# Performance work log

Measured on AMD Instinct MI355X. Metric: run time of the kernel, lower is better.

The kernel has to match this reference:

```python
import jax, jax.numpy as jnp
import numpy as np
from jax import lax

C = 96          # channels (d_model)
D_STATE = 16
D_CONV = 4
EXPAND = 2
D_INNER = EXPAND * C          # 192
DT_RANK = (C + 15) // 16      # 6 (ceil(d_model/16), mamba_ssm default)
B, H, W = 4, 96, 96
LN_EPS = 1e-5


def setup_inputs() -> dict:
    key = jax.random.key(0)
    ks = jax.random.split(key, 10)
    s = 0.02
    return {
        "spatial_feat": jax.random.normal(ks[0], (B, C, H, W), jnp.float32),
        "freq_feat":    jax.random.normal(ks[1], (B, C, H, W), jnp.float32),
        # fusion proj: nn.Linear(2C, C) with bias
        "proj_w": jax.random.normal(ks[2], (C, 2 * C), jnp.float32) * s,
        "proj_b": jnp.zeros((C,), jnp.float32),
        # Mamba params (mamba_ssm defaults: in/x/out proj bias=False, conv bias=True)
        "in_proj_w": jax.random.normal(ks[3], (2 * D_INNER, C), jnp.float32) * s,
        "conv_w": jax.random.normal(ks[4], (D_INNER, 1, D_CONV), jnp.float32) * s,
        "conv_b": jnp.zeros((D_INNER,), jnp.float32),
        "x_proj_w": jax.random.normal(ks[5], (DT_RANK + 2 * D_STATE, D_INNER), jnp.float32) * s,
        "dt_proj_w": jax.random.normal(ks[6], (D_INNER, DT_RANK), jnp.float32) * s,
        "dt_proj_b": jnp.full((D_INNER,), -4.6, jnp.float32),  # softplus ~ 0.01
        "A_log": jnp.log(jnp.tile(jnp.arange(1, D_STATE + 1, dtype=jnp.float32), (D_INNER, 1))),
        "D_param": jnp.ones((D_INNER,), jnp.float32),
        "out_proj_w": jax.random.normal(ks[7], (C, D_INNER), jnp.float32) * s,
        "ln_g": jnp.ones((C,), jnp.float32),
        "ln_b": jnp.zeros((C,), jnp.float32),
    }


def _mamba_fusion(spatial_feat, freq_feat, proj_w, proj_b, in_proj_w, conv_w,
                  conv_b, x_proj_w, dt_proj_w, dt_proj_b, A_log, D_param,
                  out_proj_w, ln_g, ln_b):
    Bsz, Ch, Hh, Ww = spatial_feat.shape
    L = Hh * Ww
    # concat + flatten(2).transpose(1,2): [B, L, 2C]
    seq = jnp.concatenate([spatial_feat, freq_feat], axis=1).reshape(Bsz, 2 * Ch, L).transpose(0, 2, 1)
    x = seq @ proj_w.T + proj_b  # [B, L, C]

    # ---- Mamba mixer ----
    xz = x @ in_proj_w.T                      # [B, L, 2*d_inner]
    x_in, z = jnp.split(xz, 2, axis=-1)
    # causal depthwise conv1d over sequence
    xc = lax.conv_general_dilated(
        x_in.transpose(0, 2, 1), conv_w, (1,), [(D_CONV - 1, 0)],
        dimension_numbers=('NCH', 'OIH', 'NCH'), feature_group_count=D_INNER)
    xc = jax.nn.silu(xc + conv_b[None, :, None]).transpose(0, 2, 1)  # [B, L, d_inner]

    x_dbl = xc @ x_proj_w.T                   # [B, L, dt_rank + 2*d_state]
    dt, Bm, Cm = jnp.split(x_dbl, [DT_RANK, DT_RANK + D_STATE], axis=-1)
    delta = jax.nn.softplus(dt @ dt_proj_w.T + dt_proj_b)  # [B, L, d_inner]
    A = -jnp.exp(A_log)                       # [d_inner, d_state]

    def step(h, inp):
        d_t, B_t, C_t, x_t = inp              # [B,d_in],[B,ds],[B,ds],[B,d_in]
        h = jnp.exp(d_t[:, :, None] * A) * h + (d_t * x_t)[:, :, None] * B_t[:, None, :]
        y_t = jnp.einsum('bds,bs->bd', h, C_t)
        return h, y_t

    xs = (delta.transpose(1, 0, 2), Bm.transpose(1, 0, 2),
          Cm.transpose(1, 0, 2), xc.transpose(1, 0, 2))
    h0 = jnp.zeros((Bsz, D_INNER, D_STATE), x.dtype)
    _, ys = lax.scan(step, h0, xs)            # ys: [L, B, d_inner]
    y = ys.transpose(1, 0, 2) + xc * D_param
    y = y * jax.nn.silu(z)
    mixed = y @ out_proj_w.T                  # [B, L, C]

    # LayerNorm over channel dim
    mu = mixed.mean(-1, keepdims=True)
    var = mixed.var(-1, keepdims=True)
    normed = (mixed - mu) * lax.rsqrt(var + LN_EPS) * ln_g + ln_b

    fused = normed.transpose(0, 2, 1).reshape(Bsz, Ch, Hh, Ww)
    return fused + spatial_feat


def reference(spatial_feat, freq_feat, proj_w, proj_b, in_proj_w, conv_w,
              conv_b, x_proj_w, dt_proj_w, dt_proj_b, A_log, D_param,
              out_proj_w, ln_g, ln_b):
    return _mamba_fusion(spatial_feat, freq_feat, proj_w, proj_b, in_proj_w,
                         conv_w, conv_b, x_proj_w, dt_proj_w, dt_proj_b,
                         A_log, D_param, out_proj_w, ln_g, ln_b)
```

## Files before the change

### kernel.cpp

```cpp
#include <hip/hip_runtime.h>
#include <math.h>

#define kC    96
#define kL    9216
#define kB    4
#define kDI   192
#define kDS   16
#define kDTR  6
#define kCL   128
#define kNC   72
#define kNROW (kB*kL)
#define kNSEQ (kB*kDI*kDS)

__device__ __forceinline__ float silu_f(float v) { return v / (1.f + expf(-v)); }

__global__ __launch_bounds__(256)
void k0_prep(const float* __restrict__ proj_w, const float* __restrict__ proj_b,
             const float* __restrict__ in_proj_w, const float* __restrict__ A_log,
             float* __restrict__ WcT, float* __restrict__ bias_c, float* __restrict__ A)
{
    int idx = blockIdx.x * 256 + threadIdx.x;
    if (idx < 384 * 192) {
        int co = idx / 192;
        int k  = idx % 192;
        float acc = 0.f;
        #pragma unroll 4
        for (int c = 0; c < 96; ++c)
            acc += in_proj_w[co * 96 + c] * proj_w[c * 192 + k];
        WcT[k * 384 + co] = acc;
    }
    if (idx < 384) {
        float acc = 0.f;
        for (int c = 0; c < 96; ++c) acc += in_proj_w[idx * 96 + c] * proj_b[c];
        bias_c[idx] = acc;
    }
    if (idx < kDI * kDS) {
        A[idx] = -expf(A_log[idx]);
    }
}

__global__ __launch_bounds__(384)
void k1_xz(const float* __restrict__ spatial, const float* __restrict__ freq,
           const float* __restrict__ WcT, const float* __restrict__ bias_c,
           float* __restrict__ x_in, float* __restrict__ z)
{
    __shared__ float sq[192 * 16];
    const int t   = threadIdx.x;
    const int blk = blockIdx.x;
    const int b   = blk / (kL / 16);
    const int l0  = (blk % (kL / 16)) * 16;

    #pragma unroll
    for (int i = 0; i < 8; ++i) {
        int e  = i * 384 + t;
        int k  = e >> 4, li = e & 15;
        float v;
        if (k < 96) v = spatial[(size_t)(b * 96 + k) * kL + l0 + li];
        else        v = freq   [(size_t)(b * 96 + (k - 96)) * kL + l0 + li];
        sq[e] = v;
    }
    __syncthreads();

    const int co = t;
    float acc[16];
    {
        float bc = bias_c[co];
        #pragma unroll
        for (int i = 0; i < 16; ++i) acc[i] = bc;
    }
    const float4* sq4 = (const float4*)sq;
    const float* wp = WcT + co;
    for (int k = 0; k < 192; ++k) {
        float w = wp[k * 384];
        float4 a0 = sq4[k * 4 + 0];
        float4 a1 = sq4[k * 4 + 1];
        float4 a2 = sq4[k * 4 + 2];
        float4 a3 = sq4[k * 4 + 3];
        acc[0]  += w * a0.x;  acc[1]  += w * a0.y;  acc[2]  += w * a0.z;  acc[3]  += w * a0.w;
        acc[4]  += w * a1.x;  acc[5]  += w * a1.y;  acc[6]  += w * a1.z;  acc[7]  += w * a1.w;
        acc[8]  += w * a2.x;  acc[9]  += w * a2.y;  acc[10] += w * a2.z;  acc[11] += w * a2.w;
        acc[12] += w * a3.x;  acc[13] += w * a3.y;  acc[14] += w * a3.z;  acc[15] += w * a3.w;
    }
    const size_t rbase = (size_t)b * kL + l0;
    if (co < 192) {
        #pragma unroll
        for (int li = 0; li < 16; ++li) x_in[(rbase + li) * 192 + co] = acc[li];
    } else {
        #pragma unroll
        for (int li = 0; li < 16; ++li) z[(rbase + li) * 192 + (co - 192)] = acc[li];
    }
}

__global__ __launch_bounds__(256)
void k2_conv(const float* __restrict__ x_in, const float* __restrict__ conv_w,
             const float* __restrict__ conv_b, float* __restrict__ xc)
{
    int idx = blockIdx.x * 256 + threadIdx.x;
    if (idx >= kNROW * 48) return;
    const int d4 = idx % 48;
    const int r  = idx / 48;
    const int l  = r % kL;
    const int d0 = d4 * 4;
    float ax = 0.f, ay = 0.f, az = 0.f, aw = 0.f;
    #pragma unroll
    for (int k = 0; k < 4; ++k) {
        int li = l - 3 + k;
        if (li < 0) continue;
        const float4 xv = *(const float4*)&x_in[(size_t)(r - 3 + k) * 192 + d0];
        ax += xv.x * conv_w[(d0 + 0) * 4 + k];
        ay += xv.y * conv_w[(d0 + 1) * 4 + k];
        az += xv.z * conv_w[(d0 + 2) * 4 + k];
        aw += xv.w * conv_w[(d0 + 3) * 4 + k];
    }
    float4 o;
    o.x = silu_f(ax + conv_b[d0 + 0]);
    o.y = silu_f(ay + conv_b[d0 + 1]);
    o.z = silu_f(az + conv_b[d0 + 2]);
    o.w = silu_f(aw + conv_b[d0 + 3]);
    *(float4*)&xc[(size_t)r * 192 + d0] = o;
}

__global__ __launch_bounds__(256)
void k3_xproj(const float* __restrict__ xc, const float* __restrict__ x_proj_w,
              float* __restrict__ dtr, float* __restrict__ BC)
{
    int idx = blockIdx.x * 256 + threadIdx.x;
    if (idx >= kNROW * 38) return;
    const int j = idx % 38;
    const int r = idx / 38;
    const float4* xr = (const float4*)&xc[(size_t)r * 192];
    const float4* wr = (const float4*)&x_proj_w[j * 192];
    float acc = 0.f;
    #pragma unroll 4
    for (int k4 = 0; k4 < 48; ++k4) {
        float4 a = xr[k4], w = wr[k4];
        acc += a.x * w.x + a.y * w.y + a.z * w.z + a.w * w.w;
    }
    if (j < 6) dtr[(size_t)r * 6 + j] = acc;
    else       BC[(size_t)r * 32 + (j - 6)] = acc;
}

__global__ __launch_bounds__(256)
void k4_dt(const float* __restrict__ dtr, const float* __restrict__ dt_proj_w,
           const float* __restrict__ dt_proj_b, float* __restrict__ delta)
{
    int idx = blockIdx.x * 256 + threadIdx.x;
    if (idx >= kNROW * 192) return;
    const int d = idx % 192;
    const int r = idx / 192;
    float acc = dt_proj_b[d];
    #pragma unroll
    for (int j = 0; j < 6; ++j)
        acc += dtr[(size_t)r * 6 + j] * dt_proj_w[d * 6 + j];
    float sp = (acc > 20.f) ? acc : log1pf(expf(acc));
    delta[(size_t)r * 192 + d] = sp;
}

__global__ __launch_bounds__(256)
void k5_scan1(const float* __restrict__ delta, const float* __restrict__ xc,
              const float* __restrict__ BC, const float* __restrict__ A,
              float* __restrict__ Pc, float* __restrict__ Sc)
{
    const int wid  = (blockIdx.x * 256 + threadIdx.x) >> 6;
    const int lane = threadIdx.x & 63;
    const int c  = wid % kNC;
    const int dg = (wid / kNC) % 48;
    const int b  = wid / (kNC * 48);
    const int s  = lane & 15;
    const int d  = dg * 4 + (lane >> 4);
    const float Ads = A[dg * 64 + lane];

    const size_t rbase = (size_t)b * kL + (size_t)c * kCL;
    const float* dp = delta + rbase * 192 + d;
    const float* xp = xc    + rbase * 192 + d;
    const float* bp = BC    + rbase * 32  + s;

    float P = 1.f, S = 0.f;
    #pragma unroll 4
    for (int i = 0; i < kCL; ++i) {
        float dv = *dp, xv = *xp, bv = *bp;
        float a  = __expf(dv * Ads);
        float bt = dv * xv * bv;
        P *= a;
        S  = a * S + bt;
        dp += 192; xp += 192; bp += 32;
    }
    const int row = (b * 192 + d) * 16 + s;
    Pc[(size_t)c * kNSEQ + row] = P;
    Sc[(size_t)c * kNSEQ + row] = S;
}

__global__ __launch_bounds__(256)
void k6_cscan(const float* __restrict__ Pc, const float* __restrict__ Sc,
              float* __restrict__ hin)
{
    const int row = blockIdx.x * 256 + threadIdx.x;
    float h = 0.f;
    for (int c = 0; c < kNC; ++c) {
        size_t o = (size_t)c * kNSEQ + row;
        hin[o] = h;
        h = Pc[o] * h + Sc[o];
    }
}

__global__ __launch_bounds__(256)
void k7_scan2(const float* __restrict__ delta, const float* __restrict__ xc,
              const float* __restrict__ BC, const float* __restrict__ A,
              const float* __restrict__ hin, float* __restrict__ ys)
{
    const int wid  = (blockIdx.x * 256 + threadIdx.x) >> 6;
    const int lane = threadIdx.x & 63;
    const int c  = wid % kNC;
    const int dg = (wid / kNC) % 48;
    const int b  = wid / (kNC * 48);
    const int s  = lane & 15;
    const int d  = dg * 4 + (lane >> 4);
    const float Ads = A[dg * 64 + lane];
    const int row = (b * 192 + d) * 16 + s;

    const size_t rbase = (size_t)b * kL + (size_t)c * kCL;
    const float* dp = delta + rbase * 192 + d;
    const float* xp = xc    + rbase * 192 + d;
    const float* bp = BC    + rbase * 32  + s;
    const float* cp = BC    + rbase * 32  + 16 + s;
    float*       yp = ys    + rbase * 192 + d;

    float h = hin[(size_t)c * kNSEQ + row];
    for (int i = 0; i < kCL; ++i) {
        float dv = *dp, xv = *xp, bv = *bp, cv = *cp;
        float a = __expf(dv * Ads);
        h = a * h + dv * xv * bv;
        float pv = h * cv;
        pv += __shfl_xor(pv, 1);
        pv += __shfl_xor(pv, 2);
        pv += __shfl_xor(pv, 4);
        pv += __shfl_xor(pv, 8);
        if (s == 0) *yp = pv;
        dp += 192; xp += 192; bp += 32; cp += 32; yp += 192;
    }
}

__global__ __launch_bounds__(256)
void k8_final(const float* __restrict__ ys, const float* __restrict__ xc,
              const float* __restrict__ z, const float* __restrict__ Dp,
              const float* __restrict__ out_proj_w, const float* __restrict__ ln_g,
              const float* __restrict__ ln_b, const float* __restrict__ spatial,
              float* __restrict__ out)
{
    __shared__ float yt[32 * 196];
    __shared__ float wt[96 * 36];
    const int t = threadIdx.x;
    const size_t r0 = (size_t)blockIdx.x * 32;
    const int b = (int)(r0 / kL);

    #pragma unroll
    for (int i = 0; i < 6; ++i) {
        int e  = i * 256 + t;
        int l  = e / 48, d4 = e % 48;
        size_t r = r0 + l;
        float4 yv = *(const float4*)&ys[r * 192 + d4 * 4];
        float4 xv = *(const float4*)&xc[r * 192 + d4 * 4];
        float4 zv = *(const float4*)&z [r * 192 + d4 * 4];
        float4 Dv = *(const float4*)&Dp[d4 * 4];
        float4 o;
        o.x = (yv.x + xv.x * Dv.x) * silu_f(zv.x);
        o.y = (yv.y + xv.y * Dv.y) * silu_f(zv.y);
        o.z = (yv.z + xv.z * Dv.z) * silu_f(zv.z);
        o.w = (yv.w + xv.w * Dv.w) * silu_f(zv.w);
        *(float4*)&yt[l * 196 + d4 * 4] = o;
    }
    __syncthreads();

    const int l  = t >> 3;
    const int cg = t & 7;
    float acc[12];
    #pragma unroll
    for (int i = 0; i < 12; ++i) acc[i] = 0.f;

    for (int kc = 0; kc < 6; ++kc) {
        __syncthreads();
        #pragma unroll
        for (int i = 0; i < 3; ++i) {
            int e = i * 256 + t;
            int c = e / 8, k4 = e % 8;
            float4 w = *(const float4*)&out_proj_w[c * 192 + kc * 32 + k4 * 4];
            *(float4*)&wt[c * 36 + k4 * 4] = w;
        }
        __syncthreads();
        #pragma unroll
        for (int k4 = 0; k4 < 8; ++k4) {
            float4 yv = *(const float4*)&yt[l * 196 + kc * 32 + k4 * 4];
            #pragma unroll
            for (int i = 0; i < 12; ++i) {
                const float4 wv = *(const float4*)&wt[(cg + 8 * i) * 36 + k4 * 4];
                acc[i] += yv.x * wv.x + yv.y * wv.y + yv.z * wv.z + yv.w * wv.w;
            }
        }
    }

    float sum = 0.f, ss = 0.f;
    #pragma unroll
    for (int i = 0; i < 12; ++i) { sum += acc[i]; ss += acc[i] * acc[i]; }
    #pragma unroll
    for (int m = 1; m < 8; m <<= 1) {
        sum += __shfl_xor(sum, m);
        ss  += __shfl_xor(ss, m);
    }
    const float mu  = sum * (1.f / 96.f);
    const float var = ss * (1.f / 96.f) - mu * mu;
    const float rs  = rsqrtf(var + 1e-5f);
    const int lg = (int)(r0 % kL) + l;
    #pragma unroll
    for (int i = 0; i < 12; ++i) {
        int c = cg + 8 * i;
        float nv = (acc[i] - mu) * rs * ln_g[c] + ln_b[c];
        size_t o = ((size_t)b * 96 + c) * kL + lg;
        out[o] = nv + spatial[o];
    }
}

extern "C" void kernel_launch(void* const* d_in, const int* in_sizes, int n_in,
                              void* d_out, int out_size, void* d_ws, size_t ws_size,
                              hipStream_t stream) {
    const float* spatial    = (const float*)d_in[0];
    const float* freq       = (const float*)d_in[1];
    const float* proj_w     = (const float*)d_in[2];
    const float* proj_b     = (const float*)d_in[3];
    const float* in_proj_w  = (const float*)d_in[4];
    const float* conv_w     = (const float*)d_in[5];
    const float* conv_b     = (const float*)d_in[6];
    const float* x_proj_w   = (const float*)d_in[7];
    const float* dt_proj_w  = (const float*)d_in[8];
    const float* dt_proj_b  = (const float*)d_in[9];
    const float* A_log      = (const float*)d_in[10];
    const float* D_param    = (const float*)d_in[11];
    const float* out_proj_w = (const float*)d_in[12];
    const float* ln_g       = (const float*)d_in[13];
    const float* ln_b       = (const float*)d_in[14];
    float* out = (float*)d_out;

    char* wsb = (char*)d_ws;
    size_t off = 0;
    auto alloc = [&](size_t bytes) -> float* {
        float* p = (float*)(wsb + off);
        off += (bytes + 255) & ~(size_t)255;
        return p;
    };
    float* x_in  = alloc((size_t)kNROW * kDI * 4);
    float* z     = alloc((size_t)kNROW * kDI * 4);
    float* xc    = alloc((size_t)kNROW * kDI * 4);
    float* delta = alloc((size_t)kNROW * kDI * 4);
    float* dtr   = alloc((size_t)kNROW * kDTR * 4);
    float* BC    = alloc((size_t)kNROW * 32 * 4);
    float* Pc    = alloc((size_t)kNC * kNSEQ * 4);
    float* Sc    = alloc((size_t)kNC * kNSEQ * 4);
    float* hin   = alloc((size_t)kNC * kNSEQ * 4);
    float* WcT   = alloc((size_t)192 * 384 * 4);
    float* biasc = alloc(384 * 4);
    float* Aa    = alloc((size_t)kDI * kDS * 4);
    float* ys    = x_in;

    k0_prep <<<288,  256, 0, stream>>>(proj_w, proj_b, in_proj_w, A_log, WcT, biasc, Aa);
    k1_xz   <<<2304, 384, 0, stream>>>(spatial, freq, WcT, biasc, x_in, z);
    k2_conv <<<6912, 256, 0, stream>>>(x_in, conv_w, conv_b, xc);
    k3_xproj<<<5472, 256, 0, stream>>>(xc, x_proj_w, dtr, BC);
    k4_dt   <<<27648,256, 0, stream>>>(dtr, dt_proj_w, dt_proj_b, delta);
    k5_scan1<<<3456, 256, 0, stream>>>(delta, xc, BC, Aa, Pc, Sc);
    k6_cscan<<<48,   256, 0, stream>>>(Pc, Sc, hin);
    k7_scan2<<<3456, 256, 0, stream>>>(delta, xc, BC, Aa, hin, ys);
    k8_final<<<1152, 256, 0, stream>>>(ys, xc, z, D_param, out_proj_w, ln_g, ln_b, spatial, out);
}
```

Before: 664.8 us.

## Fuse x_proj and dt_proj kernels and retile the input projection GEMM

Merges the x_proj and dt_proj/softplus kernels into one block-tiled kernel. It stages 64 rows of xc transposed in shared memory, keeps dt_rank values on chip instead of writing a dtr buffer, and reuses the same shared tile to transpose delta for coalesced stores. The k1 input-projection GEMM is retiled to 32 rows per block and 6x8 register accumulators per thread with float4 staging loads, which raises reuse per weight load. Trade-offs: larger shared-memory footprint and far fewer blocks (576) for the fused kernel, which may reduce occupancy and latency hiding.

```diff
diff --git a/kernel.cpp b/kernel.cpp
--- a/kernel.cpp
+++ b/kernel.cpp
@@ -39,55 +39,66 @@
     }
 }
 
-__global__ __launch_bounds__(384)
+__global__ __launch_bounds__(256)
 void k1_xz(const float* __restrict__ spatial, const float* __restrict__ freq,
            const float* __restrict__ WcT, const float* __restrict__ bias_c,
            float* __restrict__ x_in, float* __restrict__ z)
 {
-    __shared__ float sq[192 * 16];
+    __shared__ float As[192 * 36];
     const int t   = threadIdx.x;
     const int blk = blockIdx.x;
-    const int b   = blk / (kL / 16);
-    const int l0  = (blk % (kL / 16)) * 16;
-
-    #pragma unroll
-    for (int i = 0; i < 8; ++i) {
-        int e  = i * 384 + t;
-        int k  = e >> 4, li = e & 15;
-        float v;
-        if (k < 96) v = spatial[(size_t)(b * 96 + k) * kL + l0 + li];
-        else        v = freq   [(size_t)(b * 96 + (k - 96)) * kL + l0 + li];
-        sq[e] = v;
+    const int b   = blk / 288;
+    const int l0  = (blk % 288) * 32;
+
+    #pragma unroll
+    for (int i = 0; i < 6; ++i) {
+        int e  = i * 256 + t;
+        int k  = e >> 3, lg = e & 7;
+        const float* src = (k < 96)
+            ? &spatial[(size_t)(b * 96 + k) * kL]
+            : &freq   [(size_t)(b * 96 + (k - 96)) * kL];
+        float4 v = *(const float4*)&src[l0 + lg * 4];
+        *(float4*)&As[k * 36 + lg * 4] = v;
     }
     __syncthreads();
 
-    const int co = t;
-    float acc[16];
-    {
-        float bc = bias_c[co];
-        #pragma unroll
-        for (int i = 0; i < 16; ++i) acc[i] = bc;
-    }
-    const float4* sq4 = (const float4*)sq;
-    const float* wp = WcT + co;
+    const int w    = t >> 6;
+    const int lane = t & 63;
+    float acc[6][8];
+    #pragma unroll
+    for (int i = 0; i < 6; ++i) {
+        float bc = bias_c[lane + 64 * i];
+        #pragma unroll
+        for (int l = 0; l < 8; ++l) acc[i][l] = bc;
+    }
+
+    const float* wp = WcT + lane;
+    #pragma unroll 2
     for (int k = 0; k < 192; ++k) {
-        float w = wp[k * 384];
-        float4 a0 = sq4[k * 4 + 0];
-        float4 a1 = sq4[k * 4 + 1];
-        float4 a2 = sq4[k * 4 + 2];
-        float4 a3 = sq4[k * 4 + 3];
-        acc[0]  += w * a0.x;  acc[1]  += w * a0.y;  acc[2]  += w * a0.z;  acc[3]  += w * a0.w;
-        acc[4]  += w * a1.x;  acc[5]  += w * a1.y;  acc[6]  += w * a1.z;  acc[7]  += w * a1.w;
-        acc[8]  += w * a2.x;  acc[9]  += w * a2.y;  acc[10] += w * a2.z;  acc[11] += w * a2.w;
-        acc[12] += w * a3.x;  acc[13] += w * a3.y;  acc[14] += w * a3.z;  acc[15] += w * a3.w;
-    }
-    const size_t rbase = (size_t)b * kL + l0;
-    if (co < 192) {
-        #pragma unroll
-        for (int li = 0; li < 16; ++li) x_in[(rbase + li) * 192 + co] = acc[li];
-    } else {
-        #pragma unroll
-        for (int li = 0; li < 16; ++li) z[(rbase + li) * 192 + (co - 192)] = acc[li];
+        const float4 a0 = *(const float4*)&As[k * 36 + w * 8];
+        const float4 a1 = *(const float4*)&As[k * 36 + w * 8 + 4];
+        float wv[6];
+        #pragma unroll
+        for (int i = 0; i < 6; ++i) wv[i] = wp[k * 384 + 64 * i];
+        #pragma unroll
+        for (int i = 0; i < 6; ++i) {
+            acc[i][0] += wv[i] * a0.x;  acc[i][1] += wv[i] * a0.y;
+            acc[i][2] += wv[i] * a0.z;  acc[i][3] += wv[i] * a0.w;
+            acc[i][4] += wv[i] * a1.x;  acc[i][5] += wv[i] * a1.y;
+            acc[i][6] += wv[i] * a1.z;  acc[i][7] += wv[i] * a1.w;
+        }
+    }
+
+    const size_t rbase = (size_t)b * kL + l0 + w * 8;
+    #pragma unroll
+    for (int l = 0; l < 8; ++l) {
+        const size_t ro = (rbase + l) * 192;
+        #pragma unroll
+        for (int i = 0; i < 3; ++i)
+            x_in[ro + lane + 64 * i] = acc[i][l];
+        #pragma unroll
+        for (int i = 3; i < 6; ++i)
+            z[ro + lane + 64 * i - 192] = acc[i][l];
     }
 }
 
@@ -121,39 +132,93 @@
 }
 
 __global__ __launch_bounds__(256)
-void k3_xproj(const float* __restrict__ xc, const float* __restrict__ x_proj_w,
-              float* __restrict__ dtr, float* __restrict__ BC)
-{
-    int idx = blockIdx.x * 256 + threadIdx.x;
-    if (idx >= kNROW * 38) return;
-    const int j = idx % 38;
-    const int r = idx / 38;
-    const float4* xr = (const float4*)&xc[(size_t)r * 192];
-    const float4* wr = (const float4*)&x_proj_w[j * 192];
-    float acc = 0.f;
+void k34(const float* __restrict__ xc, const float* __restrict__ x_proj_w,
+         const float* __restrict__ dt_proj_w, const float* __restrict__ dt_proj_b,
+         float* __restrict__ BC, float* __restrict__ delta)
+{
+    __shared__ float xcT[192 * 65];
+    __shared__ float bc_s[64 * 33];
+    __shared__ float dtr_s[64 * 9];
+    const int t = threadIdx.x;
+    const size_t R0 = (size_t)blockIdx.x * 64;
+
+    #pragma unroll
+    for (int i = 0; i < 12; ++i) {
+        int e = i * 256 + t;
+        int r = e / 48, k4 = e % 48;
+        float4 v = *(const float4*)&xc[(R0 + r) * 192 + k4 * 4];
+        xcT[(k4 * 4 + 0) * 65 + r] = v.x;
+        xcT[(k4 * 4 + 1) * 65 + r] = v.y;
+        xcT[(k4 * 4 + 2) * 65 + r] = v.z;
+        xcT[(k4 * 4 + 3) * 65 + r] = v.w;
+    }
+    __syncthreads();
+
+    const int lane = t & 63;
+    const int w = __builtin_amdgcn_readfirstlane(t >> 6);
+
+    float acc[10];
+    #pragma unroll
+    for (int i = 0; i < 10; ++i) acc[i] = 0.f;
+    int jj[10];
+    #pragma unroll
+    for (int i = 0; i < 10; ++i) { int j = w + 4 * i; jj[i] = (j < 38) ? j : 37; }
+
     #pragma unroll 4
-    for (int k4 = 0; k4 < 48; ++k4) {
-        float4 a = xr[k4], w = wr[k4];
-        acc += a.x * w.x + a.y * w.y + a.z * w.z + a.w * w.w;
-    }
-    if (j < 6) dtr[(size_t)r * 6 + j] = acc;
-    else       BC[(size_t)r * 32 + (j - 6)] = acc;
-}
-
-__global__ __launch_bounds__(256)
-void k4_dt(const float* __restrict__ dtr, const float* __restrict__ dt_proj_w,
-           const float* __restrict__ dt_proj_b, float* __restrict__ delta)
-{
-    int idx = blockIdx.x * 256 + threadIdx.x;
-    if (idx >= kNROW * 192) return;
-    const int d = idx % 192;
-    const int r = idx / 192;
-    float acc = dt_proj_b[d];
-    #pragma unroll
-    for (int j = 0; j < 6; ++j)
-        acc += dtr[(size_t)r * 6 + j] * dt_proj_w[d * 6 + j];
-    float sp = (acc > 20.f) ? acc : log1pf(expf(acc));
-    delta[(size_t)r * 192 + d] = sp;
+    for (int k = 0; k < 192; ++k) {
+        const float xv = xcT[k * 65 + lane];
+        #pragma unroll
+        for (int i = 0; i < 10; ++i)
+            acc[i] += xv * x_proj_w[jj[i] * 192 + k];
+    }
+
+    #pragma unroll
+    for (int i = 0; i < 10; ++i) {
+        int j = w + 4 * i;
+        if (j < 6)       dtr_s[lane * 9 + j] = acc[i];
+        else if (j < 38) bc_s[lane * 33 + (j - 6)] = acc[i];
+    }
+    __syncthreads();
+
+    #pragma unroll
+    for (int i = 0; i < 2; ++i) {
+        int e = i * 256 + t;
+        int r = e >> 3, j4 = e & 7;
+        float4 v;
+        v.x = bc_s[r * 33 + j4 * 4 + 0];
+        v.y = bc_s[r * 33 + j4 * 4 + 1];
+        v.z = bc_s[r * 33 + j4 * 4 + 2];
+        v.w = bc_s[r * 33 + j4 * 4 + 3];
+        *(float4*)&BC[(R0 + r) * 32 + j4 * 4] = v;
+    }
+
+    {
+        float dtv[6];
+        #pragma unroll
+        for (int j = 0; j < 6; ++j) dtv[j] = dtr_s[lane * 9 + j];
+        #pragma unroll 4
+        for (int m = 0; m < 48; ++m) {
+            const int d = w * 48 + m;
+            float a = dt_proj_b[d];
+            #pragma unroll
+            for (int j = 0; j < 6; ++j) a += dtv[j] * dt_proj_w[d * 6 + j];
+            float sp = (a > 20.f) ? a : log1pf(expf(a));
+            xcT[d * 65 + lane] = sp;
+        }
+    }
+    __syncthreads();
+
+    #pragma unroll
+    for (int i = 0; i < 12; ++i) {
+        int e = i * 256 + t;
+        int r = e / 48, d4 = e % 48;
+        float4 v;
+        v.x = xcT[(d4 * 4 + 0) * 65 + r];
+        v.y = xcT[(d4 * 4 + 1) * 65 + r];
+        v.z = xcT[(d4 * 4 + 2) * 65 + r];
+        v.w = xcT[(d4 * 4 + 3) * 65 + r];
+        *(float4*)&delta[(R0 + r) * 192 + d4 * 4] = v;
+    }
 }
 
 __global__ __launch_bounds__(256)
@@ -350,7 +415,6 @@
     float* z     = alloc((size_t)kNROW * kDI * 4);
     float* xc    = alloc((size_t)kNROW * kDI * 4);
     float* delta = alloc((size_t)kNROW * kDI * 4);
-    float* dtr   = alloc((size_t)kNROW * kDTR * 4);
     float* BC    = alloc((size_t)kNROW * 32 * 4);
     float* Pc    = alloc((size_t)kNC * kNSEQ * 4);
     float* Sc    = alloc((size_t)kNC * kNSEQ * 4);
@@ -361,10 +425,9 @@
     float* ys    = x_in;
 
     k0_prep <<<288,  256, 0, stream>>>(proj_w, proj_b, in_proj_w, A_log, WcT, biasc, Aa);
-    k1_xz   <<<2304, 384, 0, stream>>>(spatial, freq, WcT, biasc, x_in, z);
+    k1_xz   <<<1152, 256, 0, stream>>>(spatial, freq, WcT, biasc, x_in, z);
     k2_conv <<<6912, 256, 0, stream>>>(x_in, conv_w, conv_b, xc);
-    k3_xproj<<<5472, 256, 0, stream>>>(xc, x_proj_w, dtr, BC);
-    k4_dt   <<<27648,256, 0, stream>>>(dtr, dt_proj_w, dt_proj_b, delta);
+    k34     <<<576,  256, 0, stream>>>(xc, x_proj_w, dt_proj_w, dt_proj_b, BC, delta);
     k5_scan1<<<3456, 256, 0, stream>>>(delta, xc, BC, Aa, Pc, Sc);
     k6_cscan<<<48,   256, 0, stream>>>(Pc, Sc, hin);
     k7_scan2<<<3456, 256, 0, stream>>>(delta, xc, BC, Aa, hin, ys);
```

Measured after the change: 557.3 us. 16.2% less time.
